# Optimization experiments

Hardware: AMD Instinct MI355X
Metric: run time of the kernel (lower is better)

Reference implementation:

```python
import jax, jax.numpy as jnp
import numpy as np

B = 32          # batch (decoding sequences)
HID = 4096      # hidden_size
NH = 32         # num query heads
NKV = 8         # num kv heads
HS = 128        # head_size
BS = 16         # paged-cache block size
MAXS = 2048     # max context length
MAXB = MAXS // BS            # blocks per sequence
NBLOCKS = B * MAXB           # total cache blocks
ROPE_BASE = 10000.0


def rope(x, pos):
    # NeoX rotate-half RoPE (offset = head_size//2, rotary_ndims = head_size).
    # x: [T, n_head, HS], pos: [T] int
    half = x.shape[-1] // 2
    inv_freq = 1.0 / (ROPE_BASE ** (jnp.arange(half, dtype=jnp.float32) * 2.0 / (2 * half)))
    freqs = pos[:, None].astype(jnp.float32) * inv_freq[None, :]   # [T, half]
    cos = jnp.cos(freqs)[:, None, :]
    sin = jnp.sin(freqs)[:, None, :]
    x1, x2 = x[..., :half], x[..., half:]
    return jnp.concatenate([x1 * cos - x2 * sin, x2 * cos + x1 * sin], axis=-1)


def setup_inputs() -> dict:
    key = jax.random.key(0)
    ks = jax.random.split(key, 8)
    hidden_states = jax.random.normal(ks[0], (B, 1, HID), jnp.float32)
    wq = jax.random.normal(ks[1], (NH * HS, HID), jnp.float32) * 0.02
    wk = jax.random.normal(ks[2], (NKV * HS, HID), jnp.float32) * 0.02
    wv = jax.random.normal(ks[3], (NKV * HS, HID), jnp.float32) * 0.02
    wo = jax.random.normal(ks[4], (NH * HS, NH * HS), jnp.float32) * 0.02
    k_cache = jax.random.normal(ks[5], (NBLOCKS, BS, NKV, HS), jnp.float32)
    v_cache = jax.random.normal(ks[6], (NBLOCKS, BS, NKV, HS), jnp.float32)
    # each sequence owns a disjoint set of MAXB blocks
    block_tables = jnp.arange(NBLOCKS, dtype=jnp.int32).reshape(B, MAXB)
    input_lengths = jax.random.randint(ks[7], (B,), 1, MAXS + 1, jnp.int32)
    position_ids = (input_lengths - 1).astype(jnp.int64)  # decode: write at last position
    last = input_lengths - 1
    slots = (block_tables[jnp.arange(B), last // BS] * BS + last % BS).astype(jnp.int32)
    return {
        "hidden_states": hidden_states, "wq": wq, "wk": wk, "wv": wv, "wo": wo,
        "k_cache": k_cache, "v_cache": v_cache, "position_ids": position_ids,
        "block_tables": block_tables, "slots": slots,
        "input_lengths": input_lengths, "max_s": MAXS,
    }


def reference(hidden_states, wq, wk, wv, wo, k_cache, v_cache,
              position_ids, block_tables, slots, input_lengths, max_s):
    bsz, q_len, hid = hidden_states.shape
    x = hidden_states.reshape(bsz * q_len, hid)
    q = (x @ wq.T).reshape(-1, NH, HS)
    k = (x @ wk.T).reshape(-1, NKV, HS)
    v = (x @ wv.T).reshape(-1, NKV, HS)
    q = rope(q, position_ids)
    k = rope(k, position_ids)
    # reshape_and_cache: scatter rope'd k and v into paged cache at slot indices
    kc = k_cache.reshape(-1, NKV, HS).at[slots].set(k)   # [NBLOCKS*BS, NKV, HS]
    vc = v_cache.reshape(-1, NKV, HS).at[slots].set(v)
    # single-query paged attention: gather per-sequence K/V via block_tables
    flat_idx = (block_tables[:, :, None] * BS
                + jnp.arange(BS, dtype=block_tables.dtype)[None, None, :]).reshape(bsz, -1)  # [B, max_s]
    keys = kc[flat_idx]    # [B, S, NKV, HS]
    vals = vc[flat_idx]    # [B, S, NKV, HS]
    groups = NH // NKV
    qg = q.reshape(bsz, NKV, groups, HS)
    scale = HS ** -0.5
    scores = jnp.einsum('bhgd,bshd->bhgs', qg, keys) * scale       # [B, NKV, G, S]
    valid = jnp.arange(max_s)[None, :] < input_lengths[:, None]    # [B, S]
    scores = jnp.where(valid[:, None, None, :], scores, -jnp.inf)
    p = jax.nn.softmax(scores, axis=-1)
    attn = jnp.einsum('bhgs,bshd->bhgd', p, vals).reshape(bsz, NH * HS)
    return (attn @ wo.T).reshape(bsz, q_len, hid)
```

## Files before the change

### kernel.cpp

```cpp
#include <hip/hip_runtime.h>
#include <math.h>


typedef __attribute__((ext_vector_type(8))) short bf16x8;
typedef __attribute__((ext_vector_type(4))) float f32x4;

__device__ __forceinline__ unsigned short f2bf(float f) {
    unsigned int u = __float_as_uint(f);
    return (unsigned short)((u + 0x7FFFu + ((u >> 16) & 1u)) >> 16);
}
__device__ __forceinline__ bf16x8 cvt8(float4 a, float4 b) {
    bf16x8 r;
    r[0] = (short)f2bf(a.x); r[1] = (short)f2bf(a.y);
    r[2] = (short)f2bf(a.z); r[3] = (short)f2bf(a.w);
    r[4] = (short)f2bf(b.x); r[5] = (short)f2bf(b.y);
    r[6] = (short)f2bf(b.z); r[7] = (short)f2bf(b.w);
    return r;
}

__device__ __forceinline__ void mfma_block(
    const float* __restrict__ xp, const float* __restrict__ wp,
    float* __restrict__ dst, int dstr, int n0, int mh)
{
    __shared__ float red[4][64][4];
    int wave = threadIdx.x >> 6, lane = threadIdx.x & 63;
    f32x4 acc = {0.f, 0.f, 0.f, 0.f};
#pragma unroll 4
    for (int s = 0; s < 32; ++s) {
        float4 xa = *(const float4*)(xp + s * 32);
        float4 xb = *(const float4*)(xp + s * 32 + 4);
        float4 wa = *(const float4*)(wp + s * 32);
        float4 wb = *(const float4*)(wp + s * 32 + 4);
        acc = __builtin_amdgcn_mfma_f32_16x16x32_bf16(
            cvt8(xa, xb), cvt8(wa, wb), acc, 0, 0, 0);
    }
    red[wave][lane][0] = acc[0];
    red[wave][lane][1] = acc[1];
    red[wave][lane][2] = acc[2];
    red[wave][lane][3] = acc[3];
    __syncthreads();
    if (threadIdx.x < 64) {
        int l = threadIdx.x;
        int ccol = n0 + (l & 15);
        int rbase = mh * 16 + ((l >> 4) << 2);
#pragma unroll
        for (int j = 0; j < 4; ++j) {
            float s = red[0][l][j] + red[1][l][j] + red[2][l][j] + red[3][l][j];
            dst[(size_t)(rbase + j) * dstr + ccol] = s;
        }
    }
}

__global__ __launch_bounds__(256) void qkv_mfma(
    const float* __restrict__ x, const float* __restrict__ wq,
    const float* __restrict__ wk, const float* __restrict__ wv,
    float* __restrict__ qb, float* __restrict__ knb, float* __restrict__ vnb)
{
    int tb = blockIdx.x;
    int mh = tb & 1, nt = tb >> 1;
    int wave = threadIdx.x >> 6, lane = threadIdx.x & 63;
    const float* w; float* dst; int dstr; int n0;
    if (nt < 256)      { w = wq; n0 = nt * 16;         dst = qb;  dstr = 4096; }
    else if (nt < 320) { w = wk; n0 = (nt - 256) * 16; dst = knb; dstr = 1024; }
    else               { w = wv; n0 = (nt - 320) * 16; dst = vnb; dstr = 1024; }
    int row = lane & 15, kq = (lane >> 4) << 3;
    int kbase = wave << 10;
    const float* xp = x + (size_t)(mh * 16 + row) * 4096 + kbase + kq;
    const float* wp = w + (size_t)(n0 + row) * 4096 + kbase + kq;
    mfma_block(xp, wp, dst, dstr, n0, mh);
}

__global__ __launch_bounds__(256) void wo_mfma(
    const float* __restrict__ attn, const float* __restrict__ wo,
    float* __restrict__ out)
{
    int tb = blockIdx.x;
    int mh = tb & 1, nt = tb >> 1;
    int wave = threadIdx.x >> 6, lane = threadIdx.x & 63;
    int n0 = nt * 16;
    int row = lane & 15, kq = (lane >> 4) << 3;
    int kbase = wave << 10;
    const float* xp = attn + (size_t)(mh * 16 + row) * 4096 + kbase + kq;
    const float* wp = wo + (size_t)(n0 + row) * 4096 + kbase + kq;
    mfma_block(xp, wp, out, 4096, n0, mh);
}

__global__ void rope_kernel(float* __restrict__ qb, float* __restrict__ knb,
                            const int* __restrict__ lens)
{
    int bid = blockIdx.x;
    int b = bid / 40, r = bid % 40;
    float* row = (r < 32) ? (qb + (size_t)b * 4096 + r * 128)
                          : (knb + (size_t)b * 1024 + (r - 32) * 128);
    int d = threadIdx.x;
    float pos = (float)(lens[b] - 1);
    float inv = exp2f(-(float)d * 0.207620505930460f);
    float fr = pos * inv;
    float s, c;
    sincosf(fr, &s, &c);
    float x1 = row[d], x2 = row[d + 64];
    row[d]      = x1 * c - x2 * s;
    row[d + 64] = x2 * c + x1 * s;
}

#define MUL4(V, S) { V.x *= S; V.y *= S; V.z *= S; V.w *= S; }
#define FMA4(O, P, V) { O.x = fmaf(P, V.x, O.x); O.y = fmaf(P, V.y, O.y); \
                        O.z = fmaf(P, V.z, O.z); O.w = fmaf(P, V.w, O.w); }
#define DOT8(S, QA, QB, K0, K1) { \
    S = fmaf(QA.x, K0.x, S); S = fmaf(QA.y, K0.y, S); \
    S = fmaf(QA.z, K0.z, S); S = fmaf(QA.w, K0.w, S); \
    S = fmaf(QB.x, K1.x, S); S = fmaf(QB.y, K1.y, S); \
    S = fmaf(QB.z, K1.z, S); S = fmaf(QB.w, K1.w, S); }
#define RED16(X) { X += __shfl_xor(X, 1, 64); X += __shfl_xor(X, 2, 64); \
                   X += __shfl_xor(X, 4, 64); X += __shfl_xor(X, 8, 64); }
#define REDG_SUM(X) { X += __shfl_xor(X, 16, 64); X += __shfl_xor(X, 32, 64); }
#define REDG_MAX(X) { X = fmaxf(X, __shfl_xor(X, 16, 64)); \
                      X = fmaxf(X, __shfl_xor(X, 32, 64)); }
#define REDG_SUM4(V) { REDG_SUM(V.x) REDG_SUM(V.y) REDG_SUM(V.z) REDG_SUM(V.w) }

#define ALOADR(S, r_) { \
    int sl = ss[((r_) << 2) + g]; \
    const float* kp; const float* vp; \
    if (sl < 0) { kp = knew; vp = vnew; } \
    else { kp = kc + (size_t)sl * 1024 + hoff; vp = vc + (size_t)sl * 1024 + hoff; } \
    S##k0 = *(const float4*)(kp + isl); S##k1 = *(const float4*)(kp + isl + 4); \
    S##v0 = *(const float4*)(vp + isl); S##v1 = *(const float4*)(vp + isl + 4); }

#define OUPD(s_, m_, l_, Oa_, Ob_, V0_, V1_, vld_) { \
    if (s_ > m_) { \
        float c_ = __expf(m_ - s_); \
        l_ *= c_; MUL4(Oa_, c_) MUL4(Ob_, c_) \
        m_ = s_; \
    } \
    float pe_ = vld_ ? __expf(s_ - m_) : 0.f; \
    l_ += pe_; \
    FMA4(Oa_, pe_, V0_) FMA4(Ob_, pe_, V1_) }

#define ACOMP(S, r_) { \
    float s0 = 0.f, s1 = 0.f, s2 = 0.f, s3 = 0.f; \
    DOT8(s0, q0a, q0b, S##k0, S##k1) \
    DOT8(s1, q1a, q1b, S##k0, S##k1) \
    DOT8(s2, q2a, q2b, S##k0, S##k1) \
    DOT8(s3, q3a, q3b, S##k0, S##k1) \
    RED16(s0) RED16(s1) RED16(s2) RED16(s3) \
    int vld = (((r_) << 2) + g) < pend; \
    if (!vld) { s0 = s1 = s2 = s3 = -INFINITY; } \
    OUPD(s0, m0, l0, o0a, o0b, S##v0, S##v1, vld) \
    OUPD(s1, m1, l1, o1a, o1b, S##v0, S##v1, vld) \
    OUPD(s2, m2, l2, o2a, o2b, S##v0, S##v1, vld) \
    OUPD(s3, m3, l3, o3a, o3b, S##v0, S##v1, vld) }

__global__ __launch_bounds__(512, 1) void attn_kernel(
    const float* __restrict__ kc, const float* __restrict__ vc,
    const float* __restrict__ qb, const float* __restrict__ knb,
    const float* __restrict__ vnb,
    const int* __restrict__ btab, const int* __restrict__ lens,
    float* __restrict__ part)
{
    int bid = blockIdx.x;
    int c = bid >> 5, b = bid & 31;
    int len = lens[b];
    int p0 = c << 7;
    if (p0 >= len) return;
    int pend = min(len - p0, 128);
    int nr = (pend + 3) >> 2;
    int last = len - 1;

    __shared__ int ss[128];

    int t = threadIdx.x;
    int h = t >> 6;
    int lane = t & 63;
    int g = lane >> 4;
    int isl = (lane & 15) << 3;
    int hoff = h * 128;

    if (t < 64) {
        int idx = t << 1;
        int p = p0 + idx;
        int bt = btab[b * 128 + (p >> 4)];
        int base = bt * 16 + (p & 15);
        ss[idx]     = (p     == last) ? -1 : base;
        ss[idx + 1] = (p + 1 == last) ? -1 : base + 1;
    }
    __syncthreads();

    const float* knew = knb + ((size_t)b * 8 + h) * 128;
    const float* vnew = vnb + ((size_t)b * 8 + h) * 128;

    const float scale = 0.08838834764831845f;
    const float* qrow = qb + (size_t)b * 4096 + (size_t)h * 512;
    float4 q0a = *(const float4*)(qrow + isl),       q0b = *(const float4*)(qrow + isl + 4);
    float4 q1a = *(const float4*)(qrow + 128 + isl), q1b = *(const float4*)(qrow + 128 + isl + 4);
    float4 q2a = *(const float4*)(qrow + 256 + isl), q2b = *(const float4*)(qrow + 256 + isl + 4);
    float4 q3a = *(const float4*)(qrow + 384 + isl), q3b = *(const float4*)(qrow + 384 + isl + 4);
    MUL4(q0a, scale) MUL4(q0b, scale) MUL4(q1a, scale) MUL4(q1b, scale)
    MUL4(q2a, scale) MUL4(q2b, scale) MUL4(q3a, scale) MUL4(q3b, scale)

    float m0 = -INFINITY, m1 = -INFINITY, m2 = -INFINITY, m3 = -INFINITY;
    float l0 = 0.f, l1 = 0.f, l2 = 0.f, l3 = 0.f;
    float4 o0a = {0,0,0,0}, o0b = {0,0,0,0}, o1a = {0,0,0,0}, o1b = {0,0,0,0};
    float4 o2a = {0,0,0,0}, o2b = {0,0,0,0}, o3a = {0,0,0,0}, o3b = {0,0,0,0};

    float4 ak0, ak1, av0, av1;
    float4 bk0, bk1, bv0, bv1;
    float4 ck0, ck1, cv0, cv1;
    ALOADR(a, 0)
    if (1 < nr) ALOADR(b, 1)
    if (2 < nr) ALOADR(c, 2)
    for (int r = 0; r < nr; r += 3) {
        ACOMP(a, r)
        if (r + 3 < nr) ALOADR(a, r + 3)
        if (r + 1 >= nr) break;
        ACOMP(b, r + 1)
        if (r + 4 < nr) ALOADR(b, r + 4)
        if (r + 2 >= nr) break;
        ACOMP(c, r + 2)
        if (r + 5 < nr) ALOADR(c, r + 5)
    }

    float M0 = m0, M1 = m1, M2 = m2, M3 = m3;
    REDG_MAX(M0) REDG_MAX(M1) REDG_MAX(M2) REDG_MAX(M3)
    float w0 = __expf(m0 - M0), w1 = __expf(m1 - M1);
    float w2 = __expf(m2 - M2), w3 = __expf(m3 - M3);
    float L0 = w0 * l0, L1 = w1 * l1, L2 = w2 * l2, L3 = w3 * l3;
    REDG_SUM(L0) REDG_SUM(L1) REDG_SUM(L2) REDG_SUM(L3)
    MUL4(o0a, w0) MUL4(o0b, w0) MUL4(o1a, w1) MUL4(o1b, w1)
    MUL4(o2a, w2) MUL4(o2b, w2) MUL4(o3a, w3) MUL4(o3b, w3)
    REDG_SUM4(o0a) REDG_SUM4(o0b) REDG_SUM4(o1a) REDG_SUM4(o1b)
    REDG_SUM4(o2a) REDG_SUM4(o2b) REDG_SUM4(o3a) REDG_SUM4(o3b)

    float* pgb = part + (size_t)(((b * 8 + h) * 16 + c) * 4) * 132;
    if (lane < 16) {
        *(float4*)(pgb +       isl) = o0a; *(float4*)(pgb +       isl + 4) = o0b;
        *(float4*)(pgb + 132 + isl) = o1a; *(float4*)(pgb + 132 + isl + 4) = o1b;
        *(float4*)(pgb + 264 + isl) = o2a; *(float4*)(pgb + 264 + isl + 4) = o2b;
        *(float4*)(pgb + 396 + isl) = o3a; *(float4*)(pgb + 396 + isl + 4) = o3b;
    }
    if (lane == 0) {
        pgb[128] = M0; pgb[129] = L0;
        pgb[260] = M1; pgb[261] = L1;
        pgb[392] = M2; pgb[393] = L2;
        pgb[524] = M3; pgb[525] = L3;
    }
}

__global__ __launch_bounds__(256) void combine_kernel(
    const float* __restrict__ part, const int* __restrict__ lens,
    float* __restrict__ attn)
{
    int b = blockIdx.x >> 3, h = blockIdx.x & 7;
    int t = threadIdx.x;
    int g = t >> 6, lane = t & 63;
    int len = lens[b];
    int nch = (len + 127) >> 7;
    const float* base = part + (size_t)(b * 8 + h) * 8448 + (size_t)g * 132;
    float M = -INFINITY;
    for (int cc = 0; cc < nch; ++cc)
        M = fmaxf(M, base[(size_t)cc * 528 + 128]);
    float denom = 0.f, a0 = 0.f, a1 = 0.f;
    int d0 = lane << 1;
    for (int cc = 0; cc < nch; ++cc) {
        const float* pg = base + (size_t)cc * 528;
        float w = __expf(pg[128] - M);
        denom += w * pg[129];
        a0 += w * pg[d0];
        a1 += w * pg[d0 + 1];
    }
    float inv = 1.f / denom;
    float* dst = attn + (size_t)b * 4096 + (size_t)(h * 4 + g) * 128 + d0;
    dst[0] = a0 * inv;
    dst[1] = a1 * inv;
}

extern "C" void kernel_launch(void* const* d_in, const int* in_sizes, int n_in,
                              void* d_out, int out_size, void* d_ws, size_t ws_size,
                              hipStream_t stream)
{
    const float* x   = (const float*)d_in[0];
    const float* wq  = (const float*)d_in[1];
    const float* wk  = (const float*)d_in[2];
    const float* wv  = (const float*)d_in[3];
    const float* wo  = (const float*)d_in[4];
    const float* kc  = (const float*)d_in[5];
    const float* vc  = (const float*)d_in[6];
    const int* btab  = (const int*)d_in[8];
    const int* lens  = (const int*)d_in[10];

    float* qb   = (float*)d_ws;
    float* knb  = qb  + 32 * 4096;
    float* vnb  = knb + 32 * 1024;
    float* attn = vnb + 32 * 1024;
    float* part = attn + 32 * 4096;
    float* outp = (float*)d_out;

    qkv_mfma<<<768, 256, 0, stream>>>(x, wq, wk, wv, qb, knb, vnb);
    rope_kernel<<<32 * 40, 64, 0, stream>>>(qb, knb, lens);
    attn_kernel<<<512, 512, 0, stream>>>(kc, vc, qb, knb, vnb, btab, lens, part);
    combine_kernel<<<256, 256, 0, stream>>>(part, lens, attn);
    wo_mfma<<<512, 256, 0, stream>>>(attn, wo, outp);
}
```

Before: 164.5 us.

## Fuse RoPE into attention, share weight tiles across batch halves in GEMMs

Removes the standalone RoPE kernel. RoPE is now applied to q and to the new key inside the attention kernel, using a shared-memory cos/sin table and lane shuffles. The new token is handled as a separate tail step rather than through a slot-index redirect. The QKV and output-projection GEMMs now use 512-thread blocks that cover all 32 batch rows, so each converted weight fragment feeds two MFMAs and weight reads are no longer duplicated across blocks. The attention prefetch depth drops from three stages to two, and bf16 conversion now uses the library intrinsic.

```diff
diff --git a/kernel.cpp b/kernel.cpp
--- a/kernel.cpp
+++ b/kernel.cpp
@@ -1,106 +1,93 @@
 #include <hip/hip_runtime.h>
+#include <hip/hip_bf16.h>
 #include <math.h>
 
 
 typedef __attribute__((ext_vector_type(8))) short bf16x8;
 typedef __attribute__((ext_vector_type(4))) float f32x4;
 
-__device__ __forceinline__ unsigned short f2bf(float f) {
-    unsigned int u = __float_as_uint(f);
-    return (unsigned short)((u + 0x7FFFu + ((u >> 16) & 1u)) >> 16);
+__device__ __forceinline__ short f2bfs(float f) {
+    __hip_bfloat16 h = __float2bfloat16(f);
+    unsigned short u;
+    __builtin_memcpy(&u, &h, 2);
+    return (short)u;
 }
 __device__ __forceinline__ bf16x8 cvt8(float4 a, float4 b) {
     bf16x8 r;
-    r[0] = (short)f2bf(a.x); r[1] = (short)f2bf(a.y);
-    r[2] = (short)f2bf(a.z); r[3] = (short)f2bf(a.w);
-    r[4] = (short)f2bf(b.x); r[5] = (short)f2bf(b.y);
-    r[6] = (short)f2bf(b.z); r[7] = (short)f2bf(b.w);
+    r[0] = f2bfs(a.x); r[1] = f2bfs(a.y); r[2] = f2bfs(a.z); r[3] = f2bfs(a.w);
+    r[4] = f2bfs(b.x); r[5] = f2bfs(b.y); r[6] = f2bfs(b.z); r[7] = f2bfs(b.w);
     return r;
 }
 
-__device__ __forceinline__ void mfma_block(
-    const float* __restrict__ xp, const float* __restrict__ wp,
-    float* __restrict__ dst, int dstr, int n0, int mh)
-{
-    __shared__ float red[4][64][4];
+__device__ __forceinline__ void mfma_block8(
+    const float* __restrict__ xp0, const float* __restrict__ xp1,
+    const float* __restrict__ wp, float* __restrict__ dst, int dstr, int n0)
+{
+    __shared__ float red[8][64][8];
     int wave = threadIdx.x >> 6, lane = threadIdx.x & 63;
-    f32x4 acc = {0.f, 0.f, 0.f, 0.f};
+    f32x4 acc0 = {0.f, 0.f, 0.f, 0.f};
+    f32x4 acc1 = {0.f, 0.f, 0.f, 0.f};
 #pragma unroll 4
-    for (int s = 0; s < 32; ++s) {
-        float4 xa = *(const float4*)(xp + s * 32);
-        float4 xb = *(const float4*)(xp + s * 32 + 4);
-        float4 wa = *(const float4*)(wp + s * 32);
-        float4 wb = *(const float4*)(wp + s * 32 + 4);
-        acc = __builtin_amdgcn_mfma_f32_16x16x32_bf16(
-            cvt8(xa, xb), cvt8(wa, wb), acc, 0, 0, 0);
-    }
-    red[wave][lane][0] = acc[0];
-    red[wave][lane][1] = acc[1];
-    red[wave][lane][2] = acc[2];
-    red[wave][lane][3] = acc[3];
+    for (int s = 0; s < 16; ++s) {
+        float4 wa  = *(const float4*)(wp  + s * 32);
+        float4 wb  = *(const float4*)(wp  + s * 32 + 4);
+        float4 x0a = *(const float4*)(xp0 + s * 32);
+        float4 x0b = *(const float4*)(xp0 + s * 32 + 4);
+        float4 x1a = *(const float4*)(xp1 + s * 32);
+        float4 x1b = *(const float4*)(xp1 + s * 32 + 4);
+        bf16x8 wf = cvt8(wa, wb);
+        acc0 = __builtin_amdgcn_mfma_f32_16x16x32_bf16(cvt8(x0a, x0b), wf, acc0, 0, 0, 0);
+        acc1 = __builtin_amdgcn_mfma_f32_16x16x32_bf16(cvt8(x1a, x1b), wf, acc1, 0, 0, 0);
+    }
+#pragma unroll
+    for (int j = 0; j < 4; ++j) { red[wave][lane][j] = acc0[j]; red[wave][lane][4 + j] = acc1[j]; }
     __syncthreads();
-    if (threadIdx.x < 64) {
-        int l = threadIdx.x;
+    if (threadIdx.x < 128) {
+        int l = threadIdx.x & 63, half = threadIdx.x >> 6;
         int ccol = n0 + (l & 15);
-        int rbase = mh * 16 + ((l >> 4) << 2);
+        int rbase = half * 16 + ((l >> 4) << 2);
 #pragma unroll
         for (int j = 0; j < 4; ++j) {
-            float s = red[0][l][j] + red[1][l][j] + red[2][l][j] + red[3][l][j];
+            int e = (half << 2) + j;
+            float s = red[0][l][e] + red[1][l][e] + red[2][l][e] + red[3][l][e]
+                    + red[4][l][e] + red[5][l][e] + red[6][l][e] + red[7][l][e];
             dst[(size_t)(rbase + j) * dstr + ccol] = s;
         }
     }
 }
 
-__global__ __launch_bounds__(256) void qkv_mfma(
+__global__ __launch_bounds__(512) void qkv_mfma(
     const float* __restrict__ x, const float* __restrict__ wq,
     const float* __restrict__ wk, const float* __restrict__ wv,
     float* __restrict__ qb, float* __restrict__ knb, float* __restrict__ vnb)
 {
-    int tb = blockIdx.x;
-    int mh = tb & 1, nt = tb >> 1;
+    int nt = blockIdx.x;
     int wave = threadIdx.x >> 6, lane = threadIdx.x & 63;
     const float* w; float* dst; int dstr; int n0;
     if (nt < 256)      { w = wq; n0 = nt * 16;         dst = qb;  dstr = 4096; }
     else if (nt < 320) { w = wk; n0 = (nt - 256) * 16; dst = knb; dstr = 1024; }
     else               { w = wv; n0 = (nt - 320) * 16; dst = vnb; dstr = 1024; }
     int row = lane & 15, kq = (lane >> 4) << 3;
-    int kbase = wave << 10;
-    const float* xp = x + (size_t)(mh * 16 + row) * 4096 + kbase + kq;
-    const float* wp = w + (size_t)(n0 + row) * 4096 + kbase + kq;
-    mfma_block(xp, wp, dst, dstr, n0, mh);
-}
-
-__global__ __launch_bounds__(256) void wo_mfma(
+    int kbase = wave << 9;
+    const float* xp0 = x + (size_t)row * 4096 + kbase + kq;
+    const float* xp1 = xp0 + (size_t)16 * 4096;
+    const float* wp  = w + (size_t)(n0 + row) * 4096 + kbase + kq;
+    mfma_block8(xp0, xp1, wp, dst, dstr, n0);
+}
+
+__global__ __launch_bounds__(512) void wo_mfma(
     const float* __restrict__ attn, const float* __restrict__ wo,
     float* __restrict__ out)
 {
-    int tb = blockIdx.x;
-    int mh = tb & 1, nt = tb >> 1;
+    int nt = blockIdx.x;
     int wave = threadIdx.x >> 6, lane = threadIdx.x & 63;
     int n0 = nt * 16;
     int row = lane & 15, kq = (lane >> 4) << 3;
-    int kbase = wave << 10;
-    const float* xp = attn + (size_t)(mh * 16 + row) * 4096 + kbase + kq;
-    const float* wp = wo + (size_t)(n0 + row) * 4096 + kbase + kq;
-    mfma_block(xp, wp, out, 4096, n0, mh);
-}
-
-__global__ void rope_kernel(float* __restrict__ qb, float* __restrict__ knb,
-                            const int* __restrict__ lens)
-{
-    int bid = blockIdx.x;
-    int b = bid / 40, r = bid % 40;
-    float* row = (r < 32) ? (qb + (size_t)b * 4096 + r * 128)
-                          : (knb + (size_t)b * 1024 + (r - 32) * 128);
-    int d = threadIdx.x;
-    float pos = (float)(lens[b] - 1);
-    float inv = exp2f(-(float)d * 0.207620505930460f);
-    float fr = pos * inv;
-    float s, c;
-    sincosf(fr, &s, &c);
-    float x1 = row[d], x2 = row[d + 64];
-    row[d]      = x1 * c - x2 * s;
-    row[d + 64] = x2 * c + x1 * s;
+    int kbase = wave << 9;
+    const float* xp0 = attn + (size_t)row * 4096 + kbase + kq;
+    const float* xp1 = xp0 + (size_t)16 * 4096;
+    const float* wp  = wo + (size_t)(n0 + row) * 4096 + kbase + kq;
+    mfma_block8(xp0, xp1, wp, out, 4096, n0);
 }
 
 #define MUL4(V, S) { V.x *= S; V.y *= S; V.z *= S; V.w *= S; }
@@ -118,13 +105,30 @@
                       X = fmaxf(X, __shfl_xor(X, 32, 64)); }
 #define REDG_SUM4(V) { REDG_SUM(V.x) REDG_SUM(V.y) REDG_SUM(V.z) REDG_SUM(V.w) }
 
+#define ROPE8(A, B) { \
+    float pax = __shfl_xor(A.x, 8, 64), pay = __shfl_xor(A.y, 8, 64); \
+    float paz = __shfl_xor(A.z, 8, 64), paw = __shfl_xor(A.w, 8, 64); \
+    float pbx = __shfl_xor(B.x, 8, 64), pby = __shfl_xor(B.y, 8, 64); \
+    float pbz = __shfl_xor(B.z, 8, 64), pbw = __shfl_xor(B.w, 8, 64); \
+    int ci = (i & 7) << 3; \
+    float2 c0 = cs[ci + 0], c1 = cs[ci + 1], c2 = cs[ci + 2], c3 = cs[ci + 3]; \
+    float2 c4 = cs[ci + 4], c5 = cs[ci + 5], c6 = cs[ci + 6], c7 = cs[ci + 7]; \
+    float sg = (i < 8) ? -1.f : 1.f; \
+    A.x = fmaf(sg * pax, c0.y, A.x * c0.x); \
+    A.y = fmaf(sg * pay, c1.y, A.y * c1.x); \
+    A.z = fmaf(sg * paz, c2.y, A.z * c2.x); \
+    A.w = fmaf(sg * paw, c3.y, A.w * c3.x); \
+    B.x = fmaf(sg * pbx, c4.y, B.x * c4.x); \
+    B.y = fmaf(sg * pby, c5.y, B.y * c5.x); \
+    B.z = fmaf(sg * pbz, c6.y, B.z * c6.x); \
+    B.w = fmaf(sg * pbw, c7.y, B.w * c7.x); }
+
 #define ALOADR(S, r_) { \
     int sl = ss[((r_) << 2) + g]; \
-    const float* kp; const float* vp; \
-    if (sl < 0) { kp = knew; vp = vnew; } \
-    else { kp = kc + (size_t)sl * 1024 + hoff; vp = vc + (size_t)sl * 1024 + hoff; } \
-    S##k0 = *(const float4*)(kp + isl); S##k1 = *(const float4*)(kp + isl + 4); \
-    S##v0 = *(const float4*)(vp + isl); S##v1 = *(const float4*)(vp + isl + 4); }
+    const float* kp = kc + (size_t)sl * 1024 + hoff + isl; \
+    const float* vp = vc + (size_t)sl * 1024 + hoff + isl; \
+    S##k0 = *(const float4*)(kp); S##k1 = *(const float4*)(kp + 4); \
+    S##v0 = *(const float4*)(vp); S##v1 = *(const float4*)(vp + 4); }
 
 #define OUPD(s_, m_, l_, Oa_, Ob_, V0_, V1_, vld_) { \
     if (s_ > m_) { \
@@ -143,7 +147,7 @@
     DOT8(s2, q2a, q2b, S##k0, S##k1) \
     DOT8(s3, q3a, q3b, S##k0, S##k1) \
     RED16(s0) RED16(s1) RED16(s2) RED16(s3) \
-    int vld = (((r_) << 2) + g) < pend; \
+    int vld = (((r_) << 2) + g) < cend; \
     if (!vld) { s0 = s1 = s2 = s3 = -INFINITY; } \
     OUPD(s0, m0, l0, o0a, o0b, S##v0, S##v1, vld) \
     OUPD(s1, m1, l1, o1a, o1b, S##v0, S##v1, vld) \
@@ -162,31 +166,36 @@
     int len = lens[b];
     int p0 = c << 7;
     if (p0 >= len) return;
-    int pend = min(len - p0, 128);
-    int nr = (pend + 3) >> 2;
     int last = len - 1;
+    int cend = min(last - p0, 128);
+    int hasTail = (last - p0) < 128;
+    int nr = (cend + 3) >> 2;
 
     __shared__ int ss[128];
+    __shared__ float2 cs[64];
 
     int t = threadIdx.x;
     int h = t >> 6;
     int lane = t & 63;
     int g = lane >> 4;
-    int isl = (lane & 15) << 3;
+    int i = lane & 15;
+    int isl = i << 3;
     int hoff = h * 128;
 
     if (t < 64) {
-        int idx = t << 1;
+        float inv = exp2f(-(float)t * 0.20762050593046014f);
+        float fr = (float)last * inv;
+        float s_, c_;
+        sincosf(fr, &s_, &c_);
+        cs[t] = make_float2(c_, s_);
+    } else if (t < 128) {
+        int idx = (t - 64) << 1;
         int p = p0 + idx;
         int bt = btab[b * 128 + (p >> 4)];
-        int base = bt * 16 + (p & 15);
-        ss[idx]     = (p     == last) ? -1 : base;
-        ss[idx + 1] = (p + 1 == last) ? -1 : base + 1;
+        ss[idx]     = bt * 16 + (p & 15);
+        ss[idx + 1] = bt * 16 + (p & 15) + 1;
     }
     __syncthreads();
-
-    const float* knew = knb + ((size_t)b * 8 + h) * 128;
-    const float* vnew = vnb + ((size_t)b * 8 + h) * 128;
 
     const float scale = 0.08838834764831845f;
     const float* qrow = qb + (size_t)b * 4096 + (size_t)h * 512;
@@ -194,6 +203,7 @@
     float4 q1a = *(const float4*)(qrow + 128 + isl), q1b = *(const float4*)(qrow + 128 + isl + 4);
     float4 q2a = *(const float4*)(qrow + 256 + isl), q2b = *(const float4*)(qrow + 256 + isl + 4);
     float4 q3a = *(const float4*)(qrow + 384 + isl), q3b = *(const float4*)(qrow + 384 + isl + 4);
+    ROPE8(q0a, q0b) ROPE8(q1a, q1b) ROPE8(q2a, q2b) ROPE8(q3a, q3b)
     MUL4(q0a, scale) MUL4(q0b, scale) MUL4(q1a, scale) MUL4(q1b, scale)
     MUL4(q2a, scale) MUL4(q2b, scale) MUL4(q3a, scale) MUL4(q3b, scale)
 
@@ -202,21 +212,38 @@
     float4 o0a = {0,0,0,0}, o0b = {0,0,0,0}, o1a = {0,0,0,0}, o1b = {0,0,0,0};
     float4 o2a = {0,0,0,0}, o2b = {0,0,0,0}, o3a = {0,0,0,0}, o3b = {0,0,0,0};
 
+    if (hasTail) {
+        const float* kn = knb + ((size_t)b * 8 + h) * 128 + isl;
+        const float* vn = vnb + ((size_t)b * 8 + h) * 128 + isl;
+        float4 tk0 = *(const float4*)(kn), tk1 = *(const float4*)(kn + 4);
+        float4 tv0 = *(const float4*)(vn), tv1 = *(const float4*)(vn + 4);
+        ROPE8(tk0, tk1)
+        float s0 = 0.f, s1 = 0.f, s2 = 0.f, s3 = 0.f;
+        DOT8(s0, q0a, q0b, tk0, tk1)
+        DOT8(s1, q1a, q1b, tk0, tk1)
+        DOT8(s2, q2a, q2b, tk0, tk1)
+        DOT8(s3, q3a, q3b, tk0, tk1)
+        RED16(s0) RED16(s1) RED16(s2) RED16(s3)
+        int vld = (g == 0);
+        if (!vld) { s0 = s1 = s2 = s3 = -INFINITY; }
+        OUPD(s0, m0, l0, o0a, o0b, tv0, tv1, vld)
+        OUPD(s1, m1, l1, o1a, o1b, tv0, tv1, vld)
+        OUPD(s2, m2, l2, o2a, o2b, tv0, tv1, vld)
+        OUPD(s3, m3, l3, o3a, o3b, tv0, tv1, vld)
+    }
+
     float4 ak0, ak1, av0, av1;
     float4 bk0, bk1, bv0, bv1;
-    float4 ck0, ck1, cv0, cv1;
-    ALOADR(a, 0)
-    if (1 < nr) ALOADR(b, 1)
-    if (2 < nr) ALOADR(c, 2)
-    for (int r = 0; r < nr; r += 3) {
-        ACOMP(a, r)
-        if (r + 3 < nr) ALOADR(a, r + 3)
-        if (r + 1 >= nr) break;
-        ACOMP(b, r + 1)
-        if (r + 4 < nr) ALOADR(b, r + 4)
-        if (r + 2 >= nr) break;
-        ACOMP(c, r + 2)
-        if (r + 5 < nr) ALOADR(c, r + 5)
+    if (nr > 0) {
+        ALOADR(a, 0)
+        if (1 < nr) ALOADR(b, 1)
+        for (int r = 0; r < nr; r += 2) {
+            ACOMP(a, r)
+            if (r + 2 < nr) ALOADR(a, r + 2)
+            if (r + 1 >= nr) break;
+            ACOMP(b, r + 1)
+            if (r + 3 < nr) ALOADR(b, r + 3)
+        }
     }
 
     float M0 = m0, M1 = m1, M2 = m2, M3 = m3;
@@ -294,9 +321,8 @@
     float* part = attn + 32 * 4096;
     float* outp = (float*)d_out;
 
-    qkv_mfma<<<768, 256, 0, stream>>>(x, wq, wk, wv, qb, knb, vnb);
-    rope_kernel<<<32 * 40, 64, 0, stream>>>(qb, knb, lens);
+    qkv_mfma<<<384, 512, 0, stream>>>(x, wq, wk, wv, qb, knb, vnb);
     attn_kernel<<<512, 512, 0, stream>>>(kc, vc, qb, knb, vnb, btab, lens, part);
     combine_kernel<<<256, 256, 0, stream>>>(part, lens, attn);
-    wo_mfma<<<512, 256, 0, stream>>>(attn, wo, outp);
-}
+    wo_mfma<<<256, 512, 0, stream>>>(attn, wo, outp);
+}
```

Measured after the change: 155.5 us. 5.5% less time.
